# Kernel optimization log

Measured on AMD Instinct MI355X. Metric: run time of the kernel, lower is better.

## Reference

```python
import jax, jax.numpy as jnp
import numpy as np

DIM = 1024
HEADS = 16
HEAD_DIM = DIM // HEADS
THRESH = 0.29514
SHARP = 15.0
LN_EPS = 1e-5
NORM_EPS = 1e-12


def setup_inputs() -> dict:
    key = jax.random.key(0)
    ks = jax.random.split(key, 8)
    s = 1.0 / np.sqrt(DIM)
    sg = 1.0 / np.sqrt(HEAD_DIM)
    return {
        "x": jax.random.normal(ks[0], (2, 2048, DIM), dtype=jnp.float32),
        "Wq": jax.random.uniform(ks[1], (DIM, DIM), jnp.float32, -s, s),
        "Wk": jax.random.uniform(ks[2], (DIM, DIM), jnp.float32, -s, s),
        "Wv": jax.random.uniform(ks[3], (DIM, DIM), jnp.float32, -s, s),
        "gq": jax.random.uniform(ks[4], (HEAD_DIM,), jnp.float32, -sg, sg),
        "gk": jax.random.uniform(ks[5], (HEAD_DIM,), jnp.float32, -sg, sg),
        "Wo": jax.random.uniform(ks[6], (DIM, DIM), jnp.float32, -s, s),
        "bo": jax.random.uniform(ks[7], (DIM,), jnp.float32, -s, s),
        "ln_w": jnp.ones((DIM,), jnp.float32),
        "ln_b": jnp.zeros((DIM,), jnp.float32),
    }


def _l2norm(t):
    # F.normalize: t / max(||t||_2, eps)
    n = jnp.sqrt(jnp.sum(t * t, axis=-1, keepdims=True))
    return t / jnp.maximum(n, NORM_EPS)


def reference(x, Wq, Wk, Wv, gq, gk, Wo, bo, ln_w, ln_b):
    B, T, D = x.shape
    # LayerNorm over last dim
    mu = jnp.mean(x, axis=-1, keepdims=True)
    var = jnp.mean((x - mu) ** 2, axis=-1, keepdims=True)
    x_norm = (x - mu) / jnp.sqrt(var + LN_EPS) * ln_w + ln_b

    def split_heads(t):  # [B,T,D] -> [B,H,T,hd]
        return t.reshape(B, T, HEADS, HEAD_DIM).transpose(0, 2, 1, 3)

    q = _l2norm(split_heads(x_norm @ Wq))
    k = _l2norm(split_heads(x_norm @ Wk))
    v = split_heads(x @ Wv)  # note: v uses un-normalized x, as in source

    align = jnp.einsum("bhtd,bhsd->bhts", q, k)  # cosine alignment
    resonance = jax.nn.sigmoid((align - THRESH) * SHARP)
    gate_q = jnp.einsum("bhtd,d->bht", q, gq)
    gate_k = jnp.einsum("bhsd,d->bhs", k, gk)
    modulation = resonance * gate_q[..., :, None] * gate_k[..., None, :]
    collapse = jnp.einsum("bhts,bhsd->bhtd", modulation, v)
    collapse = collapse.transpose(0, 2, 1, 3).reshape(B, T, D)
    return collapse @ Wo + bo
```

## Files before the change

### kernel.cpp

```cpp
#include <hip/hip_runtime.h>
#include <math.h>

#define DIM 1024
#define T_SEQ 2048
#define NBATCH 2
#define HEADS 16
#define HD 64
#define NTOK 4096
#define THRESH 0.29514f
#define SHARP 15.0f
#define LOG2E 1.4426950408889634f

typedef __attribute__((ext_vector_type(8))) short bf16x8;
typedef __attribute__((ext_vector_type(4))) float f32x4;
typedef __attribute__((ext_vector_type(4))) unsigned int u32x4;

__device__ __forceinline__ unsigned short f2b(float f) {
    unsigned int u = __float_as_uint(f);
    unsigned int r = (u + 0x7FFFu + ((u >> 16) & 1u)) >> 16;
    return (unsigned short)r;
}
__device__ __forceinline__ float b2f(unsigned short u) {
    return __uint_as_float(((unsigned int)u) << 16);
}
__device__ __forceinline__ unsigned int pack2_bf16(float lo, float hi) {
    unsigned int a = __float_as_uint(lo) + 0x8000u;
    unsigned int b = __float_as_uint(hi) + 0x8000u;
    return __builtin_amdgcn_perm(b, a, 0x07060302u);
}

__device__ __forceinline__ void async_cp16(const unsigned short* g, unsigned short* l) {
    __builtin_amdgcn_global_load_lds(
        (const __attribute__((address_space(1))) unsigned int*)g,
        (__attribute__((address_space(3))) unsigned int*)l, 16, 0, 0);
}

__global__ __launch_bounds__(256) void ln_xnorm_kernel(
    const float* __restrict__ x, const float* __restrict__ lnw, const float* __restrict__ lnb,
    unsigned short* __restrict__ xnb, unsigned short* __restrict__ xb) {
    int row = blockIdx.x * 4 + (threadIdx.x >> 6);
    int lane = threadIdx.x & 63;
    const float4* xr = (const float4*)(x + (size_t)row * DIM);
    float4 v[4];
    float s = 0.f, ss = 0.f;
#pragma unroll
    for (int i = 0; i < 4; i++) {
        v[i] = xr[lane + i * 64];
        s += v[i].x + v[i].y + v[i].z + v[i].w;
        ss += v[i].x * v[i].x + v[i].y * v[i].y + v[i].z * v[i].z + v[i].w * v[i].w;
    }
#pragma unroll
    for (int off = 32; off; off >>= 1) {
        s += __shfl_xor(s, off);
        ss += __shfl_xor(ss, off);
    }
    float m = s * (1.f / DIM);
    float rstd = rsqrtf(ss * (1.f / DIM) - m * m + 1e-5f);
#pragma unroll
    for (int i = 0; i < 4; i++) {
        int e = (lane + i * 64) * 4;
        float4 lw = *(const float4*)&lnw[e];
        float4 lb = *(const float4*)&lnb[e];
        ushort4 un, ur;
        un.x = f2b((v[i].x - m) * rstd * lw.x + lb.x);
        un.y = f2b((v[i].y - m) * rstd * lw.y + lb.y);
        un.z = f2b((v[i].z - m) * rstd * lw.z + lb.z);
        un.w = f2b((v[i].w - m) * rstd * lw.w + lb.w);
        ur.x = f2b(v[i].x); ur.y = f2b(v[i].y); ur.z = f2b(v[i].z); ur.w = f2b(v[i].w);
        *(ushort4*)&xnb[(size_t)row * DIM + e] = un;
        *(ushort4*)&xb[(size_t)row * DIM + e] = ur;
    }
}

__global__ __launch_bounds__(256) void wtrans_kernel(
    const float* __restrict__ W0, const float* __restrict__ W1,
    const float* __restrict__ W2, const float* __restrict__ W3,
    unsigned short* __restrict__ T0, unsigned short* __restrict__ T1,
    unsigned short* __restrict__ T2, unsigned short* __restrict__ T3) {
    __shared__ float tile[64][65];
    const int z = blockIdx.z;
    const float* W = (z == 0) ? W0 : (z == 1) ? W1 : (z == 2) ? W2 : W3;
    unsigned short* T = (z == 0) ? T0 : (z == 1) ? T1 : (z == 2) ? T2 : T3;
    const int k0 = blockIdx.x * 64, n0 = blockIdx.y * 64;
    const int r = threadIdx.x >> 3;
    const int c = (threadIdx.x & 7) * 8;
#pragma unroll
    for (int half = 0; half < 2; half++) {
        int rr = r + half * 32;
        float4 a = *(const float4*)&W[(size_t)(k0 + rr) * DIM + n0 + c];
        float4 b = *(const float4*)&W[(size_t)(k0 + rr) * DIM + n0 + c + 4];
        tile[rr][c + 0] = a.x; tile[rr][c + 1] = a.y; tile[rr][c + 2] = a.z; tile[rr][c + 3] = a.w;
        tile[rr][c + 4] = b.x; tile[rr][c + 5] = b.y; tile[rr][c + 6] = b.z; tile[rr][c + 7] = b.w;
    }
    __syncthreads();
#pragma unroll
    for (int half = 0; half < 2; half++) {
        int dd = r + half * 32;
        bf16x8 o;
#pragma unroll
        for (int j = 0; j < 8; j++) o[j] = (short)f2b(tile[c + j][dd]);
        *(bf16x8*)&T[(size_t)(n0 + dd) * DIM + k0 + c] = o;
    }
}

template <int MODE>
__global__ __launch_bounds__(256) void gemm_mfma_kernel(
    const unsigned short* __restrict__ A0, const unsigned short* __restrict__ A2,
    const unsigned short* __restrict__ Bt0, const unsigned short* __restrict__ Bt1,
    const unsigned short* __restrict__ Bt2, const float* __restrict__ bias,
    const float* __restrict__ gq, const float* __restrict__ gk,
    unsigned short* __restrict__ Oq, unsigned short* __restrict__ Ok,
    unsigned short* __restrict__ Ov, float* __restrict__ gq_t, float* __restrict__ gk_t,
    float* __restrict__ Oout) {
    __shared__ __align__(16) unsigned short As[2][128 * 32];
    __shared__ __align__(16) unsigned short Bs[2][128 * 32];
    const int tid = threadIdx.x;
    const int lane = tid & 63, w = tid >> 6;
    const int l16 = lane & 15, quad = lane >> 4;
    const int wm = w >> 1, wn = w & 1;
    const int m0 = blockIdx.x * 128, n0 = blockIdx.y * 128;
    const unsigned short* A;
    const unsigned short* Bt;
    int z = 0;
    if constexpr (MODE == 0) {
        z = blockIdx.z;
        A = (z == 2) ? A2 : A0;
        Bt = (z == 0) ? Bt0 : (z == 1) ? Bt1 : Bt2;
    } else {
        A = A0;
        Bt = Bt0;
    }
    f32x4 acc[4][4] = {};
    const int kswz = (l16 >> 1) & 3;

    const int lin0 = tid, lin1 = 256 + tid;
    const int sm0 = lin0 >> 2, sk0 = (lin0 & 3) ^ ((sm0 >> 1) & 3);
    const int sm1 = lin1 >> 2, sk1 = (lin1 & 3) ^ ((sm1 >> 1) & 3);

    auto stage = [&](int kb, int k0) {
        async_cp16(A + (size_t)(m0 + sm0) * DIM + k0 + sk0 * 8, &As[kb][lin0 * 8]);
        async_cp16(Bt + (size_t)(n0 + sm0) * DIM + k0 + sk0 * 8, &Bs[kb][lin0 * 8]);
        async_cp16(A + (size_t)(m0 + sm1) * DIM + k0 + sk1 * 8, &As[kb][lin1 * 8]);
        async_cp16(Bt + (size_t)(n0 + sm1) * DIM + k0 + sk1 * 8, &Bs[kb][lin1 * 8]);
    };

    stage(0, 0);
    __syncthreads();

    for (int ks = 0; ks < DIM / 32; ks++) {
        const int cur = ks & 1;
        if (ks + 1 < DIM / 32) stage(cur ^ 1, (ks + 1) * 32);
        bf16x8 af[4], bfr[4];
#pragma unroll
        for (int t = 0; t < 4; t++) {
            int ma = wm * 64 + t * 16 + l16;
            af[t] = *(const bf16x8*)(&As[cur][ma * 32 + ((quad ^ kswz) * 8)]);
            int nb = wn * 64 + t * 16 + l16;
            bfr[t] = *(const bf16x8*)(&Bs[cur][nb * 32 + ((quad ^ kswz) * 8)]);
        }
#pragma unroll
        for (int mt = 0; mt < 4; mt++)
#pragma unroll
            for (int nt = 0; nt < 4; nt++)
                acc[mt][nt] =
                    __builtin_amdgcn_mfma_f32_16x16x32_bf16(af[mt], bfr[nt], acc[mt][nt], 0, 0, 0);
        __syncthreads();
    }

    if constexpr (MODE == 0) {
        const int h = (n0 + wn * 64) >> 6;
        if (z <= 1) {
            constexpr float QSCALE = -SHARP * LOG2E;
            const float* gvec = (z == 0) ? gq : gk;
            float* gate = (z == 0) ? gq_t : gk_t;
            unsigned short* O = (z == 0) ? Oq : Ok;
            const float oscale = (z == 0) ? QSCALE : 1.0f;
            float gv[4];
#pragma unroll
            for (int nt = 0; nt < 4; nt++) gv[nt] = gvec[nt * 16 + l16];
#pragma unroll
            for (int mt = 0; mt < 4; mt++) {
#pragma unroll
                for (int r = 0; r < 4; r++) {
                    float ss = 0.f;
#pragma unroll
                    for (int nt = 0; nt < 4; nt++) ss += acc[mt][nt][r] * acc[mt][nt][r];
#pragma unroll
                    for (int msk = 1; msk < 16; msk <<= 1) ss += __shfl_xor(ss, msk);
                    float rn = __builtin_amdgcn_rcpf(fmaxf(sqrtf(ss), 1e-12f));
                    float vn[4], gg = 0.f;
#pragma unroll
                    for (int nt = 0; nt < 4; nt++) {
                        vn[nt] = acc[mt][nt][r] * rn;
                        gg += vn[nt] * gv[nt];
                    }
#pragma unroll
                    for (int msk = 1; msk < 16; msk <<= 1) gg += __shfl_xor(gg, msk);
                    int tok = m0 + wm * 64 + mt * 16 + quad * 4 + r;
                    int b = tok >> 11, t = tok & 2047;
                    size_t rowbase = ((size_t)(b * HEADS + h) * T_SEQ + t) * HD;
#pragma unroll
                    for (int nt = 0; nt < 4; nt++)
                        O[rowbase + nt * 16 + l16] = f2b(vn[nt] * oscale);
                    if (l16 == 0) gate[(b * HEADS + h) * T_SEQ + t] = gg;
                }
            }
        } else {
#pragma unroll
            for (int mt = 0; mt < 4; mt++) {
#pragma unroll
                for (int r = 0; r < 4; r++) {
                    int tok = m0 + wm * 64 + mt * 16 + quad * 4 + r;
                    int b = tok >> 11, t = tok & 2047;
                    size_t rowbase = ((size_t)(b * HEADS + h) * T_SEQ + t) * HD;
#pragma unroll
                    for (int nt = 0; nt < 4; nt++)
                        Ov[rowbase + nt * 16 + l16] = f2b(acc[mt][nt][r]);
                }
            }
        }
    } else {
        float bias_r[4];
#pragma unroll
        for (int nt = 0; nt < 4; nt++) bias_r[nt] = bias[n0 + wn * 64 + nt * 16 + l16];
#pragma unroll
        for (int mt = 0; mt < 4; mt++) {
#pragma unroll
            for (int r = 0; r < 4; r++) {
                int tok = m0 + wm * 64 + mt * 16 + quad * 4 + r;
#pragma unroll
                for (int nt = 0; nt < 4; nt++) {
                    int n = n0 + wn * 64 + nt * 16 + l16;
                    Oout[(size_t)tok * DIM + n] = acc[mt][nt][r] + bias_r[nt];
                }
            }
        }
    }
}

__global__ __launch_bounds__(256) void vtrans_kernel(const unsigned short* __restrict__ Vn,
                                                     const float* __restrict__ gk_t,
                                                     unsigned short* __restrict__ Vt) {
    __shared__ float tile[64][65];
    const int bh = blockIdx.y;
    const int t0 = blockIdx.x * 64;
    const int r = threadIdx.x >> 3;
    const int c = (threadIdx.x & 7) * 8;
    const unsigned short* src = Vn + (size_t)bh * T_SEQ * HD;
#pragma unroll
    for (int half = 0; half < 2; half++) {
        int rr = r + half * 32;
        float gkv = gk_t[bh * T_SEQ + t0 + rr];
        bf16x8 v = *(const bf16x8*)(src + (size_t)(t0 + rr) * HD + c);
#pragma unroll
        for (int j = 0; j < 8; j++) tile[rr][c + j] = b2f((unsigned short)v[j]) * gkv;
    }
    __syncthreads();
    unsigned short* dst = Vt + (size_t)bh * HD * T_SEQ;
#pragma unroll
    for (int half = 0; half < 2; half++) {
        int dd = r + half * 32;
        bf16x8 o;
#pragma unroll
        for (int j = 0; j < 8; j++) o[j] = (short)f2b(tile[c + j][dd]);
        *(bf16x8*)(dst + (size_t)dd * T_SEQ + t0 + c) = o;
    }
}

__global__ __launch_bounds__(256, 4) void attn_mfma_kernel(
    const unsigned short* __restrict__ Qn, const unsigned short* __restrict__ Kn,
    const unsigned short* __restrict__ Vt, const float* __restrict__ gateq,
    unsigned short* __restrict__ collp0, unsigned short* __restrict__ collp1) {
    __shared__ __align__(16) unsigned short Ks[2][64 * 64];
    __shared__ __align__(16) unsigned short VtL[2][64 * 64];
    const int tid = threadIdx.x;
    const int lane = tid & 63, w = tid >> 6;
    const int quad = lane >> 4, l16 = lane & 15;
    const int f = blockIdx.x + 16 * blockIdx.y + 256 * blockIdx.z;
    const int q_ = f >> 3;
    const int panel = (f & 7) * 8 + (q_ >> 4);
    const int t0 = (q_ & 15) * 128;
    const int h = panel & 15;
    const int zz = panel >> 4;
    const int b = zz >> 1, shalf = zz & 1;
    const int sbase = shalf * (T_SEQ / 2);
    const int bh = b * HEADS + h;
    const size_t base = (size_t)bh * T_SEQ * HD;
    constexpr float K0 = THRESH * SHARP * LOG2E;
    const f32x4 k0v = {K0, K0, K0, K0};

    int det0 = quad, det1 = quad + 4;
    asm("v_permlane16_swap_b32 %0, %1" : "+v"(det0), "+v"(det1));
    const bool flagA = (__builtin_amdgcn_readfirstlane(det0) == 0);

    bf16x8 fq[2][2];
#pragma unroll
    for (int mt = 0; mt < 2; mt++) {
        const unsigned short* qrow = Qn + base + (size_t)(t0 + w * 32 + mt * 16 + l16) * HD;
        fq[mt][0] = *(const bf16x8*)(qrow + quad * 8);
        fq[mt][1] = *(const bf16x8*)(qrow + 32 + quad * 8);
    }

    f32x4 oacc[4][2] = {};
    const int srow = tid >> 3;
    const int sgp = tid & 7;
    const int swz = l16 & 7;

    auto stage_chunk = [&](unsigned short* ksn, unsigned short* vtn, int s0) {
#pragma unroll
        for (int half = 0; half < 2; half++) {
            int row = srow + half * 32;
            int g = sgp ^ (row & 7);
            async_cp16(Kn + base + (size_t)(s0 + row) * HD + g * 8, ksn + row * 64 + sgp * 8);
            async_cp16(Vt + base + (size_t)row * T_SEQ + s0 + g * 8, vtn + row * 64 + sgp * 8);
        }
    };

    auto do_chunk = [&](const unsigned short* ksb, const unsigned short* vtb) {
#pragma unroll
        for (int kh = 0; kh < 2; kh++) {
            unsigned int p[2][2][2];
#pragma unroll
            for (int ct2 = 0; ct2 < 2; ct2++) {
                const int ct = 2 * kh + ct2;
                const unsigned short* krow = ksb + (ct * 16 + l16) * 64;
                bf16x8 fk0 = *(const bf16x8*)(krow + (quad ^ swz) * 8);
                bf16x8 fk1 = *(const bf16x8*)(krow + ((quad + 4) ^ swz) * 8);
#pragma unroll
                for (int mt = 0; mt < 2; mt++) {
                    __builtin_amdgcn_s_setprio(1);
                    f32x4 s1 =
                        __builtin_amdgcn_mfma_f32_16x16x32_bf16(fk0, fq[mt][0], k0v, 0, 0, 0);
                    f32x4 sacc =
                        __builtin_amdgcn_mfma_f32_16x16x32_bf16(fk1, fq[mt][1], s1, 0, 0, 0);
                    __builtin_amdgcn_s_setprio(0);
                    float w0 = __builtin_amdgcn_rcpf(1.f + __builtin_amdgcn_exp2f(sacc[0]));
                    float w1 = __builtin_amdgcn_rcpf(1.f + __builtin_amdgcn_exp2f(sacc[1]));
                    float w2 = __builtin_amdgcn_rcpf(1.f + __builtin_amdgcn_exp2f(sacc[2]));
                    float w3 = __builtin_amdgcn_rcpf(1.f + __builtin_amdgcn_exp2f(sacc[3]));
                    p[mt][ct2][0] = pack2_bf16(w0, w1);
                    p[mt][ct2][1] = pack2_bf16(w2, w3);
                }
            }
            int gv = (4 * kh + 2 * (quad & 1) + (quad >> 1)) ^ swz;
            bf16x8 fv[4];
#pragma unroll
            for (int dt = 0; dt < 4; dt++)
                fv[dt] = *(const bf16x8*)(vtb + (dt * 16 + l16) * 64 + gv * 8);
#pragma unroll
            for (int mt = 0; mt < 2; mt++) {
                unsigned int aL = p[mt][0][0], aH = p[mt][0][1];
                unsigned int bL = p[mt][1][0], bH = p[mt][1][1];
                asm("v_permlane16_swap_b32 %0, %1" : "+v"(aL), "+v"(bL));
                asm("v_permlane16_swap_b32 %0, %1" : "+v"(aH), "+v"(bH));
                u32x4 bt;
                if (flagA) {
                    bt.x = aL; bt.y = aH; bt.z = bL; bt.w = bH;
                } else {
                    bt.x = bL; bt.y = bH; bt.z = aL; bt.w = aH;
                }
                bf16x8 fs = __builtin_bit_cast(bf16x8, bt);
                __builtin_amdgcn_s_setprio(1);
#pragma unroll
                for (int dt = 0; dt < 4; dt++)
                    oacc[dt][mt] =
                        __builtin_amdgcn_mfma_f32_16x16x32_bf16(fv[dt], fs, oacc[dt][mt], 0, 0, 0);
                __builtin_amdgcn_s_setprio(0);
            }
        }
        __syncthreads();
    };

    stage_chunk(&Ks[0][0], &VtL[0][0], sbase);
    __syncthreads();

    for (int j = 0; j < T_SEQ / 256; j++) {
        stage_chunk(&Ks[1][0], &VtL[1][0], sbase + j * 128 + 64);
        do_chunk(&Ks[0][0], &VtL[0][0]);
        if (j + 1 < T_SEQ / 256) stage_chunk(&Ks[0][0], &VtL[0][0], sbase + j * 128 + 128);
        do_chunk(&Ks[1][0], &VtL[1][0]);
    }

    unsigned short* collp = shalf ? collp1 : collp0;
#pragma unroll
    for (int mt = 0; mt < 2; mt++) {
        int t = t0 + w * 32 + mt * 16 + l16;
        float gq_v = gateq[bh * T_SEQ + t];
        unsigned short* dst = collp + ((size_t)b * T_SEQ + t) * DIM + h * HD;
#pragma unroll
        for (int dt = 0; dt < 4; dt++) {
            ushort4 o;
            o.x = f2b(oacc[dt][mt][0] * gq_v);
            o.y = f2b(oacc[dt][mt][1] * gq_v);
            o.z = f2b(oacc[dt][mt][2] * gq_v);
            o.w = f2b(oacc[dt][mt][3] * gq_v);
            *(ushort4*)(dst + dt * 16 + quad * 4) = o;
        }
    }
}

__global__ __launch_bounds__(256) void merge_kernel(unsigned short* __restrict__ p0,
                                                    const unsigned short* __restrict__ p1) {
    size_t i = ((size_t)blockIdx.x * 256 + threadIdx.x) * 8;
    bf16x8 a = *(const bf16x8*)(p0 + i);
    bf16x8 c = *(const bf16x8*)(p1 + i);
    bf16x8 o;
#pragma unroll
    for (int j = 0; j < 8; j++)
        o[j] = (short)f2b(b2f((unsigned short)a[j]) + b2f((unsigned short)c[j]));
    *(bf16x8*)(p0 + i) = o;
}

extern "C" void kernel_launch(void* const* d_in, const int* in_sizes, int n_in,
                              void* d_out, int out_size, void* d_ws, size_t ws_size,
                              hipStream_t stream) {
    const float* x = (const float*)d_in[0];
    const float* Wq = (const float*)d_in[1];
    const float* Wk = (const float*)d_in[2];
    const float* Wv = (const float*)d_in[3];
    const float* gq = (const float*)d_in[4];
    const float* gk = (const float*)d_in[5];
    const float* Wo = (const float*)d_in[6];
    const float* bo = (const float*)d_in[7];
    const float* lnw = (const float*)d_in[8];
    const float* lnb = (const float*)d_in[9];
    float* out = (float*)d_out;

    unsigned short* ws = (unsigned short*)d_ws;
    unsigned short* xnb = ws;
    unsigned short* xb = xnb + (size_t)NTOK * DIM;
    unsigned short* Wqt = xb + (size_t)NTOK * DIM;
    unsigned short* Wkt = Wqt + (size_t)DIM * DIM;
    unsigned short* Wvt = Wkt + (size_t)DIM * DIM;
    unsigned short* Wot = Wvt + (size_t)DIM * DIM;
    unsigned short* Q16 = Wot + (size_t)DIM * DIM;
    unsigned short* K16 = Q16 + (size_t)NTOK * DIM;
    unsigned short* Vn = K16 + (size_t)NTOK * DIM;
    float* gq_t = (float*)(Vn + (size_t)NTOK * DIM);
    float* gk_t = gq_t + NBATCH * HEADS * T_SEQ;
    unsigned short* collb1 = (unsigned short*)(gk_t + NBATCH * HEADS * T_SEQ);
    unsigned short* Vt = xnb;
    unsigned short* collb0 = xb;

    ln_xnorm_kernel<<<NTOK / 4, 256, 0, stream>>>(x, lnw, lnb, xnb, xb);
    wtrans_kernel<<<dim3(16, 16, 4), 256, 0, stream>>>(Wq, Wk, Wv, Wo, Wqt, Wkt, Wvt, Wot);
    gemm_mfma_kernel<0><<<dim3(NTOK / 128, DIM / 128, 3), 256, 0, stream>>>(
        xnb, xb, Wqt, Wkt, Wvt, nullptr, gq, gk, Q16, K16, Vn, gq_t, gk_t, nullptr);
    vtrans_kernel<<<dim3(T_SEQ / 64, NBATCH * HEADS), 256, 0, stream>>>(Vn, gk_t, Vt);
    attn_mfma_kernel<<<dim3(T_SEQ / 128, HEADS, NBATCH * 2), 256, 0, stream>>>(
        Q16, K16, Vt, gq_t, collb0, collb1);
    merge_kernel<<<(NTOK * DIM) / (256 * 8), 256, 0, stream>>>(collb0, collb1);
    gemm_mfma_kernel<1><<<dim3(NTOK / 128, DIM / 128, 1), 256, 0, stream>>>(
        collb0, nullptr, Wot, nullptr, nullptr, bo, nullptr, nullptr, nullptr, nullptr, nullptr,
        nullptr, nullptr, out);
}
```

Baseline: 216.4 us.

## Remap GEMM blocks across XCDs and use 128x64 tiles for output projection

Result: slower. 222.0 us (+2.6%).

```diff
diff --git a/kernel.cpp b/kernel.cpp
--- a/kernel.cpp
+++ b/kernel.cpp
@@ -112,25 +112,36 @@
     unsigned short* __restrict__ Oq, unsigned short* __restrict__ Ok,
     unsigned short* __restrict__ Ov, float* __restrict__ gq_t, float* __restrict__ gk_t,
     float* __restrict__ Oout) {
+    constexpr int NT = (MODE == 0) ? 4 : 2;
     __shared__ __align__(16) unsigned short As[2][128 * 32];
-    __shared__ __align__(16) unsigned short Bs[2][128 * 32];
+    __shared__ __align__(16) unsigned short Bs[2][NT * 32 * 32];
     const int tid = threadIdx.x;
     const int lane = tid & 63, w = tid >> 6;
     const int l16 = lane & 15, quad = lane >> 4;
     const int wm = w >> 1, wn = w & 1;
-    const int m0 = blockIdx.x * 128, n0 = blockIdx.y * 128;
+    int m0, n0, z = 0;
+    if constexpr (MODE == 0) {
+        const int f = blockIdx.x + (blockIdx.y << 5) + (blockIdx.z << 8);
+        const int ww = (f & 7) * 96 + (f >> 3);
+        z = ww >> 8;
+        m0 = ((ww >> 3) & 31) * 128;
+        n0 = (ww & 7) * 128;
+    } else {
+        const int f = blockIdx.x + (blockIdx.y << 5);
+        const int ww = (f & 7) * 64 + (f >> 3);
+        m0 = (ww >> 4) * 128;
+        n0 = (ww & 15) * 64;
+    }
     const unsigned short* A;
     const unsigned short* Bt;
-    int z = 0;
     if constexpr (MODE == 0) {
-        z = blockIdx.z;
         A = (z == 2) ? A2 : A0;
         Bt = (z == 0) ? Bt0 : (z == 1) ? Bt1 : Bt2;
     } else {
         A = A0;
         Bt = Bt0;
     }
-    f32x4 acc[4][4] = {};
+    f32x4 acc[4][NT] = {};
     const int kswz = (l16 >> 1) & 3;
 
     const int lin0 = tid, lin1 = 256 + tid;
@@ -139,9 +150,10 @@
 
     auto stage = [&](int kb, int k0) {
         async_cp16(A + (size_t)(m0 + sm0) * DIM + k0 + sk0 * 8, &As[kb][lin0 * 8]);
+        async_cp16(A + (size_t)(m0 + sm1) * DIM + k0 + sk1 * 8, &As[kb][lin1 * 8]);
         async_cp16(Bt + (size_t)(n0 + sm0) * DIM + k0 + sk0 * 8, &Bs[kb][lin0 * 8]);
-        async_cp16(A + (size_t)(m0 + sm1) * DIM + k0 + sk1 * 8, &As[kb][lin1 * 8]);
-        async_cp16(Bt + (size_t)(n0 + sm1) * DIM + k0 + sk1 * 8, &Bs[kb][lin1 * 8]);
+        if constexpr (MODE == 0)
+            async_cp16(Bt + (size_t)(n0 + sm1) * DIM + k0 + sk1 * 8, &Bs[kb][lin1 * 8]);
     };
 
     stage(0, 0);
@@ -150,18 +162,21 @@
     for (int ks = 0; ks < DIM / 32; ks++) {
         const int cur = ks & 1;
         if (ks + 1 < DIM / 32) stage(cur ^ 1, (ks + 1) * 32);
-        bf16x8 af[4], bfr[4];
+        bf16x8 af[4], bfr[NT];
 #pragma unroll
         for (int t = 0; t < 4; t++) {
             int ma = wm * 64 + t * 16 + l16;
             af[t] = *(const bf16x8*)(&As[cur][ma * 32 + ((quad ^ kswz) * 8)]);
-            int nb = wn * 64 + t * 16 + l16;
+        }
+#pragma unroll
+        for (int t = 0; t < NT; t++) {
+            int nb = wn * (NT * 16) + t * 16 + l16;
             bfr[t] = *(const bf16x8*)(&Bs[cur][nb * 32 + ((quad ^ kswz) * 8)]);
         }
 #pragma unroll
         for (int mt = 0; mt < 4; mt++)
 #pragma unroll
-            for (int nt = 0; nt < 4; nt++)
+            for (int nt = 0; nt < NT; nt++)
                 acc[mt][nt] =
                     __builtin_amdgcn_mfma_f32_16x16x32_bf16(af[mt], bfr[nt], acc[mt][nt], 0, 0, 0);
         __syncthreads();
@@ -220,17 +235,17 @@
             }
         }
     } else {
-        float bias_r[4];
-#pragma unroll
-        for (int nt = 0; nt < 4; nt++) bias_r[nt] = bias[n0 + wn * 64 + nt * 16 + l16];
+        float bias_r[NT];
+#pragma unroll
+        for (int nt = 0; nt < NT; nt++) bias_r[nt] = bias[n0 + wn * (NT * 16) + nt * 16 + l16];
 #pragma unroll
         for (int mt = 0; mt < 4; mt++) {
 #pragma unroll
             for (int r = 0; r < 4; r++) {
                 int tok = m0 + wm * 64 + mt * 16 + quad * 4 + r;
 #pragma unroll
-                for (int nt = 0; nt < 4; nt++) {
-                    int n = n0 + wn * 64 + nt * 16 + l16;
+                for (int nt = 0; nt < NT; nt++) {
+                    int n = n0 + wn * (NT * 16) + nt * 16 + l16;
                     Oout[(size_t)tok * DIM + n] = acc[mt][nt][r] + bias_r[nt];
                 }
             }
@@ -450,7 +465,7 @@
     attn_mfma_kernel<<<dim3(T_SEQ / 128, HEADS, NBATCH * 2), 256, 0, stream>>>(
         Q16, K16, Vt, gq_t, collb0, collb1);
     merge_kernel<<<(NTOK * DIM) / (256 * 8), 256, 0, stream>>>(collb0, collb1);
-    gemm_mfma_kernel<1><<<dim3(NTOK / 128, DIM / 128, 1), 256, 0, stream>>>(
+    gemm_mfma_kernel<1><<<dim3(NTOK / 128, DIM / 64, 1), 256, 0, stream>>>(
         collb0, nullptr, Wot, nullptr, nullptr, bo, nullptr, nullptr, nullptr, nullptr, nullptr,
         nullptr, nullptr, out);
 }
```
